# Kernel tuning notes

Measured on AMD Instinct MI355X. Metric: run time of the kernel, lower is better.

The kernel has to match this reference:

```python
import jax, jax.numpy as jnp
import numpy as np

N_NODES = 25000
N_EDGES = 400000
IN_DIM, HID_DIM, OUT_DIM = 174, 128, 64


def setup_inputs() -> dict:
    key = jax.random.key(0)
    ks = jax.random.split(key, 8)
    x = jax.random.normal(ks[0], (N_NODES, IN_DIM), dtype=jnp.float32)
    edge_index = jax.random.randint(ks[1], (2, N_EDGES), 0, N_NODES, dtype=jnp.int64)
    # PyG SAGEConv params: lin_l (neighbors, with bias), lin_r (root, no bias)
    def glorot(k, shape):
        lim = float(np.sqrt(6.0 / (shape[0] + shape[1])))
        return jax.random.uniform(k, shape, jnp.float32, -lim, lim)
    W1_l = glorot(ks[2], (HID_DIM, IN_DIM))
    W1_r = glorot(ks[3], (HID_DIM, IN_DIM))
    b1 = jnp.zeros((HID_DIM,), jnp.float32)
    W2_l = glorot(ks[4], (OUT_DIM, HID_DIM))
    W2_r = glorot(ks[5], (OUT_DIM, HID_DIM))
    b2 = jnp.zeros((OUT_DIM,), jnp.float32)
    return {"x": x, "edge_index": edge_index, "W1_l": W1_l, "b1": b1,
            "W1_r": W1_r, "W2_l": W2_l, "b2": b2, "W2_r": W2_r}


def _sage_conv(h, src, dst, W_l, b, W_r):
    # mean-aggregate neighbor features at destination nodes
    msg = h[src]                                       # [E, F] gather
    summed = jax.ops.segment_sum(msg, dst, num_segments=N_NODES)  # [N, F]
    deg = jax.ops.segment_sum(jnp.ones((src.shape[0],), h.dtype), dst,
                              num_segments=N_NODES)    # [N]
    mean = summed / jnp.maximum(deg, 1.0)[:, None]
    # out = lin_l(mean) + lin_r(h)
    return mean @ W_l.T + b + h @ W_r.T


def reference(x, edge_index, W1_l, b1, W1_r, W2_l, b2, W2_r):
    src, dst = edge_index[0], edge_index[1]
    h = _sage_conv(x, src, dst, W1_l, b1, W1_r)
    h = jax.nn.relu(h)
    # dropout is identity in eval mode (module exposes freeze() for inference)
    out = _sage_conv(h, src, dst, W2_l, b2, W2_r)
    return out
```

## Files before the change

### kernel.cpp

```cpp
#include <hip/hip_runtime.h>

#define N_NODES 25000
#define N_EDGES 400000
#define IN_DIM 174
#define HID_DIM 128
#define OUT_DIM 64
#define MPAD 25088
#define BINCAP 64

using u32 = unsigned int;
typedef __attribute__((ext_vector_type(8))) short s16x8;
typedef __attribute__((ext_vector_type(4))) float f32x4;
typedef __attribute__((ext_vector_type(4))) u32 u32x4;

__device__ __forceinline__ float bflo(u32 u) { u32 t = u << 16; return __builtin_bit_cast(float, t); }
__device__ __forceinline__ float bfhi(u32 u) { u32 t = u & 0xffff0000u; return __builtin_bit_cast(float, t); }
__device__ __forceinline__ u32 f2b(float f) {
    u32 u = __builtin_bit_cast(u32, f);
    return (u + 0x7fffu + ((u >> 16) & 1u)) >> 16;
}
__device__ __forceinline__ u32 packbf2(float a, float b) { return f2b(a) | (f2b(b) << 16); }

__device__ __forceinline__ void gload_lds16(const void* g, void* l) {
    __builtin_amdgcn_global_load_lds(
        (const __attribute__((address_space(1))) u32*)g,
        (__attribute__((address_space(3))) u32*)l, 16, 0, 0);
}

#define WB1_CNT (256 * 96)
#define WB2_CNT (128 * 64)
#define PREP_TOT (WB1_CNT + WB2_CNT + N_NODES)

__global__ __launch_bounds__(256) void prep_w_kernel(
    const float* __restrict__ W1l, const float* __restrict__ W1r,
    const float* __restrict__ W2l, const float* __restrict__ W2r,
    u32* __restrict__ wb1, u32* __restrict__ wb2, int* __restrict__ degI) {
    int idx = blockIdx.x * blockDim.x + threadIdx.x;
    if (idx < WB1_CNT) {
        int nrow = idx / 96, d2 = idx - nrow * 96;
        const float* src = (nrow < 128) ? W1l + (size_t)nrow * IN_DIM
                                        : W1r + (size_t)(nrow - 128) * IN_DIM;
        float2 v = make_float2(0.f, 0.f);
        if (d2 < 87) v = ((const float2*)src)[d2];
        wb1[idx] = packbf2(v.x, v.y);
        return;
    }
    idx -= WB1_CNT;
    if (idx < WB2_CNT) {
        int nrow = idx >> 6, d2 = idx & 63;
        const float* src = (nrow < 64) ? W2l + (size_t)nrow * HID_DIM
                                       : W2r + (size_t)(nrow - 64) * HID_DIM;
        float2 v = ((const float2*)src)[d2];
        wb2[idx] = packbf2(v.x, v.y);
        return;
    }
    idx -= WB2_CNT;
    if (idx < N_NODES) degI[idx] = 0;
}

#define G1_GEMM_BLOCKS 392
#define G1_EDGE_BLOCKS ((N_EDGES / 4 + 255) / 256)

__global__ __launch_bounds__(256) void gemm1_fused_kernel(
    const float* __restrict__ x, const ushort* __restrict__ wb1,
    ushort* __restrict__ y1n, ushort* __restrict__ y1r,
    const int* __restrict__ ei, int* __restrict__ degI, int* __restrict__ bins) {
    const int bid = blockIdx.x;
    const int tid = threadIdx.x;

    if (bid >= G1_GEMM_BLOCKS) {
        int e4 = ((bid - G1_GEMM_BLOCKS) * 256 + tid) * 4;
        if (e4 < N_EDGES) {
            int4 s = *(const int4*)(ei + e4);
            int4 t = *(const int4*)(ei + N_EDGES + e4);
            int p0 = atomicAdd(&degI[t.x], 1);
            if (p0 < BINCAP) bins[t.x * BINCAP + p0] = s.x;
            int p1 = atomicAdd(&degI[t.y], 1);
            if (p1 < BINCAP) bins[t.y * BINCAP + p1] = s.y;
            int p2 = atomicAdd(&degI[t.z], 1);
            if (p2 < BINCAP) bins[t.z * BINCAP + p2] = s.z;
            int p3 = atomicAdd(&degI[t.w], 1);
            if (p3 < BINCAP) bins[t.w * BINCAP + p3] = s.w;
        }
        return;
    }

    __shared__ ushort As[128 * 32];
    __shared__ ushort Bs[128 * 32];
    const int lane = tid & 63, w = tid >> 6;
    const int gy = bid / 196, gx = bid - gy * 196;
    const int m0 = gx * 128, n0 = gy * 128;
    const int wmo = (w >> 1) * 64;
    const int wno = (w & 1) * 64;

    f32x4 acc[4][4] = {};

    const int arow = lane >> 2;
    const int achunk = (lane & 3) * 8;
    const int r4 = tid >> 2;
    const int q  = tid & 3;

    for (int kk = 0; kk < 192; kk += 32) {
        #pragma unroll
        for (int c = 0; c < 2; ++c) {
            int r = w * 32 + c * 16;
            gload_lds16(wb1 + (size_t)(n0 + r + arow) * 192 + kk + achunk, &Bs[r * 32]);
        }
        #pragma unroll
        for (int it = 0; it < 2; ++it) {
            int r = it * 64 + r4;
            int gm = m0 + r;
            int c0 = kk + q * 8;
            u32x4 o;
            #pragma unroll
            for (int e = 0; e < 4; ++e) {
                int col = c0 + e * 2;
                float2 v = make_float2(0.f, 0.f);
                if (gm < N_NODES && col < IN_DIM)
                    v = *(const float2*)(x + (size_t)gm * IN_DIM + col);
                o[e] = packbf2(v.x, v.y);
            }
            ((u32x4*)As)[r * 4 + q] = o;
        }
        __syncthreads();
        s16x8 af[4], bf[4];
        const int fr = lane & 15, fo = (lane >> 4) * 8;
        #pragma unroll
        for (int i = 0; i < 4; ++i) {
            af[i] = *(const s16x8*)&As[(wmo + i * 16 + fr) * 32 + fo];
            bf[i] = *(const s16x8*)&Bs[(wno + i * 16 + fr) * 32 + fo];
        }
        #pragma unroll
        for (int i = 0; i < 4; ++i)
            #pragma unroll
            for (int j = 0; j < 4; ++j)
                acc[i][j] = __builtin_amdgcn_mfma_f32_16x16x32_bf16(af[i], bf[j], acc[i][j], 0, 0, 0);
        __syncthreads();
    }

    const int cr = (lane >> 4) * 4, cc = lane & 15;
    #pragma unroll
    for (int i = 0; i < 4; ++i)
        #pragma unroll
        for (int r = 0; r < 4; ++r) {
            int row = m0 + wmo + i * 16 + cr + r;
            #pragma unroll
            for (int j = 0; j < 4; ++j) {
                int colg = n0 + wno + j * 16 + cc;
                ushort* Cp = (colg < 128) ? y1n : y1r;
                int c = colg & 127;
                Cp[(size_t)row * 128 + c] = (ushort)f2b(acc[i][j][r]);
            }
        }
}

template <int K, int NSPLIT, int BM>
__global__ __launch_bounds__(256) void gemm_mfma(const ushort* __restrict__ A,
                                                 const ushort* __restrict__ B,
                                                 ushort* __restrict__ Cn,
                                                 ushort* __restrict__ Cr) {
    constexpr int MI = BM / 32;
    __shared__ ushort As[BM * 32];
    __shared__ ushort Bs[128 * 32];
    const int tid = threadIdx.x;
    const int lane = tid & 63, w = tid >> 6;
    const int m0 = blockIdx.x * BM;
    const int n0 = blockIdx.y * 128;
    const int wmo = (w >> 1) * (MI * 16);
    const int wno = (w & 1) * 64;

    f32x4 acc[MI][4] = {};

    const int arow = lane >> 2;
    const int achunk = (lane & 3) * 8;

    for (int kk = 0; kk < K; kk += 32) {
        #pragma unroll
        for (int c = 0; c < BM / 64; ++c) {
            int r = w * (BM / 4) + c * 16;
            gload_lds16(A + (size_t)(m0 + r + arow) * K + kk + achunk, &As[r * 32]);
        }
        #pragma unroll
        for (int c = 0; c < 2; ++c) {
            int r = w * 32 + c * 16;
            gload_lds16(B + (size_t)(n0 + r + arow) * K + kk + achunk, &Bs[r * 32]);
        }
        __syncthreads();
        s16x8 af[MI], bf[4];
        const int fr = lane & 15, fo = (lane >> 4) * 8;
        #pragma unroll
        for (int i = 0; i < MI; ++i)
            af[i] = *(const s16x8*)&As[(wmo + i * 16 + fr) * 32 + fo];
        #pragma unroll
        for (int j = 0; j < 4; ++j)
            bf[j] = *(const s16x8*)&Bs[(wno + j * 16 + fr) * 32 + fo];
        #pragma unroll
        for (int i = 0; i < MI; ++i)
            #pragma unroll
            for (int j = 0; j < 4; ++j)
                acc[i][j] = __builtin_amdgcn_mfma_f32_16x16x32_bf16(af[i], bf[j], acc[i][j], 0, 0, 0);
        __syncthreads();
    }

    const int cr = (lane >> 4) * 4, cc = lane & 15;
    #pragma unroll
    for (int i = 0; i < MI; ++i)
        #pragma unroll
        for (int r = 0; r < 4; ++r) {
            int row = m0 + wmo + i * 16 + cr + r;
            #pragma unroll
            for (int j = 0; j < 4; ++j) {
                int colg = n0 + wno + j * 16 + cc;
                ushort* Cp = (colg < NSPLIT) ? Cn : Cr;
                int c = (colg < NSPLIT) ? colg : colg - NSPLIT;
                Cp[(size_t)row * NSPLIT + c] = (ushort)f2b(acc[i][j][r]);
            }
        }
}

__global__ __launch_bounds__(256) void agg1_kernel(const u32* __restrict__ y1n,
                                                   const u32* __restrict__ y1r,
                                                   const int* __restrict__ degI,
                                                   const int* __restrict__ bins,
                                                   const float* __restrict__ b1,
                                                   u32* __restrict__ h1) {
    int w = threadIdx.x >> 6, lane = threadIdx.x & 63;
    int n = blockIdx.x * 4 + w;
    if (n >= N_NODES) return;
    int deg = degI[n];
    int d = min(deg, BINCAP);
    const int* bp = bins + n * BINCAP;
    float a0 = 0.f, a1 = 0.f;
    int j = 0;
    for (; j + 8 <= d; j += 8) {
        int4 sa = *(const int4*)(bp + j);
        int4 sb = *(const int4*)(bp + j + 4);
        u32 u0 = y1n[(size_t)sa.x * 64 + lane];
        u32 u1 = y1n[(size_t)sa.y * 64 + lane];
        u32 u2 = y1n[(size_t)sa.z * 64 + lane];
        u32 u3 = y1n[(size_t)sa.w * 64 + lane];
        u32 u4 = y1n[(size_t)sb.x * 64 + lane];
        u32 u5 = y1n[(size_t)sb.y * 64 + lane];
        u32 u6 = y1n[(size_t)sb.z * 64 + lane];
        u32 u7 = y1n[(size_t)sb.w * 64 + lane];
        a0 += bflo(u0) + bflo(u1) + bflo(u2) + bflo(u3)
            + bflo(u4) + bflo(u5) + bflo(u6) + bflo(u7);
        a1 += bfhi(u0) + bfhi(u1) + bfhi(u2) + bfhi(u3)
            + bfhi(u4) + bfhi(u5) + bfhi(u6) + bfhi(u7);
    }
    if (j + 4 <= d) {
        int4 s4 = *(const int4*)(bp + j);
        u32 u0 = y1n[(size_t)s4.x * 64 + lane];
        u32 u1 = y1n[(size_t)s4.y * 64 + lane];
        u32 u2 = y1n[(size_t)s4.z * 64 + lane];
        u32 u3 = y1n[(size_t)s4.w * 64 + lane];
        a0 += bflo(u0) + bflo(u1) + bflo(u2) + bflo(u3);
        a1 += bfhi(u0) + bfhi(u1) + bfhi(u2) + bfhi(u3);
        j += 4;
    }
    for (; j < d; ++j) {
        int s = bp[j];
        u32 u = y1n[(size_t)s * 64 + lane];
        a0 += bflo(u); a1 += bfhi(u);
    }
    float inv = 1.f / fmaxf((float)deg, 1.f);
    u32 ur = y1r[(size_t)n * 64 + lane];
    float2 bb = ((const float2*)b1)[lane];
    float v0 = fmaxf(a0 * inv + bflo(ur) + bb.x, 0.f);
    float v1 = fmaxf(a1 * inv + bfhi(ur) + bb.y, 0.f);
    h1[(size_t)n * 64 + lane] = packbf2(v0, v1);
}

__global__ __launch_bounds__(256) void agg2_kernel(const u32* __restrict__ y2n,
                                                   const u32* __restrict__ y2r,
                                                   const int* __restrict__ degI,
                                                   const int* __restrict__ bins,
                                                   const float* __restrict__ b2,
                                                   float2* __restrict__ out) {
    int w = threadIdx.x >> 6, lane = threadIdx.x & 63;
    int half = lane >> 5, dd = lane & 31;
    int n = blockIdx.x * 4 + w;
    if (n >= N_NODES) return;
    int deg = degI[n];
    int d = min(deg, BINCAP);
    const int* bp = bins + n * BINCAP;
    float a0 = 0.f, a1 = 0.f;
    int j = 0;
    for (; j + 8 <= d; j += 8) {
        int s0 = bp[j + half],     s1 = bp[j + 2 + half];
        int s2 = bp[j + 4 + half], s3 = bp[j + 6 + half];
        u32 u0 = y2n[(size_t)s0 * 32 + dd];
        u32 u1 = y2n[(size_t)s1 * 32 + dd];
        u32 u2 = y2n[(size_t)s2 * 32 + dd];
        u32 u3 = y2n[(size_t)s3 * 32 + dd];
        a0 += bflo(u0) + bflo(u1) + bflo(u2) + bflo(u3);
        a1 += bfhi(u0) + bfhi(u1) + bfhi(u2) + bfhi(u3);
    }
    if (j + 4 <= d) {
        int s0 = bp[j + half], s1 = bp[j + 2 + half];
        u32 u0 = y2n[(size_t)s0 * 32 + dd];
        u32 u1 = y2n[(size_t)s1 * 32 + dd];
        a0 += bflo(u0) + bflo(u1);
        a1 += bfhi(u0) + bfhi(u1);
        j += 4;
    }
    if (j + 2 <= d) {
        int s = bp[j + half];
        u32 u = y2n[(size_t)s * 32 + dd];
        a0 += bflo(u); a1 += bfhi(u);
        j += 2;
    }
    if (j < d && half == 0) {
        int s = bp[j];
        u32 u = y2n[(size_t)s * 32 + dd];
        a0 += bflo(u); a1 += bfhi(u);
    }
    a0 += __shfl_xor(a0, 32, 64);
    a1 += __shfl_xor(a1, 32, 64);
    if (half == 0) {
        float inv = 1.f / fmaxf((float)deg, 1.f);
        u32 ur = y2r[(size_t)n * 32 + dd];
        float2 bb = ((const float2*)b2)[dd];
        float2 o;
        o.x = a0 * inv + bflo(ur) + bb.x;
        o.y = a1 * inv + bfhi(ur) + bb.y;
        out[(size_t)n * 32 + dd] = o;
    }
}


extern "C" void kernel_launch(void* const* d_in, const int* in_sizes, int n_in,
                              void* d_out, int out_size, void* d_ws, size_t ws_size,
                              hipStream_t stream) {
    const float* x   = (const float*)d_in[0];
    const int*   ei  = (const int*)d_in[1];
    const float* W1l = (const float*)d_in[2];
    const float* b1  = (const float*)d_in[3];
    const float* W1r = (const float*)d_in[4];
    const float* W2l = (const float*)d_in[5];
    const float* b2  = (const float*)d_in[6];
    const float* W2r = (const float*)d_in[7];

    char* w = (char*)d_ws;
    auto alloc = [&](size_t bytes) -> char* {
        char* p = w;
        w += (bytes + 255) & ~(size_t)255;
        return p;
    };
    int* degI = (int*)alloc((size_t)N_NODES * 4);
    int* bins = (int*)alloc((size_t)N_NODES * BINCAP * 4);
    u32* wb1  = (u32*)alloc((size_t)WB1_CNT * 4);
    u32* wb2  = (u32*)alloc((size_t)WB2_CNT * 4);
    u32* y1n  = (u32*)alloc((size_t)MPAD * 64 * 4);
    u32* y1r  = (u32*)alloc((size_t)MPAD * 64 * 4);
    u32* h1   = (u32*)alloc((size_t)MPAD * 64 * 4);
    u32* y2n  = (u32*)alloc((size_t)MPAD * 32 * 4);
    u32* y2r  = (u32*)alloc((size_t)MPAD * 32 * 4);

    prep_w_kernel<<<(PREP_TOT + 255) / 256, 256, 0, stream>>>(
        W1l, W1r, W2l, W2r, wb1, wb2, degI);
    gemm1_fused_kernel<<<G1_GEMM_BLOCKS + G1_EDGE_BLOCKS, 256, 0, stream>>>(
        x, (const ushort*)wb1, (ushort*)y1n, (ushort*)y1r, ei, degI, bins);
    agg1_kernel<<<(N_NODES + 3) / 4, 256, 0, stream>>>(y1n, y1r, degI, bins, b1, h1);
    gemm_mfma<128, 64, 64><<<dim3(392, 1), 256, 0, stream>>>(
        (const ushort*)h1, (const ushort*)wb2, (ushort*)y2n, (ushort*)y2r);
    agg2_kernel<<<(N_NODES + 3) / 4, 256, 0, stream>>>(y2n, y2r, degI, bins, b2, (float2*)d_out);
}
```

Measured before the change: 80.93 us.

## Fuse layer-1 mean aggregation into the layer-2 GEMM kernel

Replaces the separate agg1 kernel and layer-2 GEMM with one kernel. Each 64-row block first gathers and averages neighbor features for its 16 rows per wave, applying bias and ReLU. It writes the bf16 result into an XOR-swizzled LDS tile, then runs the MFMA GEMM against all of W2 preloaded into LDS. This removes the h1 global round trip and one launch. The cost is much less parallelism for the latency-bound gather: 392 blocks each walking 16 nodes per wave serially, instead of thousands of one-node waves, plus 48KB of LDS per block.

```diff
diff --git a/kernel.cpp b/kernel.cpp
--- a/kernel.cpp
+++ b/kernel.cpp
@@ -90,15 +90,14 @@
     const int lane = tid & 63, w = tid >> 6;
     const int gy = bid / 196, gx = bid - gy * 196;
     const int m0 = gx * 128, n0 = gy * 128;
-    const int wmo = (w >> 1) * 64;
-    const int wno = (w & 1) * 64;
-
-    f32x4 acc[4][4] = {};
-
+    const int wmo = (w >> 1) * 64, wno = (w & 1) * 64;
     const int arow = lane >> 2;
     const int achunk = (lane & 3) * 8;
     const int r4 = tid >> 2;
     const int q  = tid & 3;
+    const int fr = lane & 15, fo = (lane >> 4) * 8;
+
+    f32x4 acc[4][4] = {};
 
     for (int kk = 0; kk < 192; kk += 32) {
         #pragma unroll
@@ -110,11 +109,10 @@
         for (int it = 0; it < 2; ++it) {
             int r = it * 64 + r4;
             int gm = m0 + r;
-            int c0 = kk + q * 8;
             u32x4 o;
             #pragma unroll
             for (int e = 0; e < 4; ++e) {
-                int col = c0 + e * 2;
+                int col = kk + q * 8 + e * 2;
                 float2 v = make_float2(0.f, 0.f);
                 if (gm < N_NODES && col < IN_DIM)
                     v = *(const float2*)(x + (size_t)gm * IN_DIM + col);
@@ -124,7 +122,6 @@
         }
         __syncthreads();
         s16x8 af[4], bf[4];
-        const int fr = lane & 15, fo = (lane >> 4) * 8;
         #pragma unroll
         for (int i = 0; i < 4; ++i) {
             af[i] = *(const s16x8*)&As[(wmo + i * 16 + fr) * 32 + fo];
@@ -154,121 +151,115 @@
         }
 }
 
-template <int K, int NSPLIT, int BM>
-__global__ __launch_bounds__(256) void gemm_mfma(const ushort* __restrict__ A,
-                                                 const ushort* __restrict__ B,
-                                                 ushort* __restrict__ Cn,
-                                                 ushort* __restrict__ Cr) {
-    constexpr int MI = BM / 32;
-    __shared__ ushort As[BM * 32];
-    __shared__ ushort Bs[128 * 32];
-    const int tid = threadIdx.x;
-    const int lane = tid & 63, w = tid >> 6;
-    const int m0 = blockIdx.x * BM;
-    const int n0 = blockIdx.y * 128;
-    const int wmo = (w >> 1) * (MI * 16);
-    const int wno = (w & 1) * 64;
-
-    f32x4 acc[MI][4] = {};
-
-    const int arow = lane >> 2;
-    const int achunk = (lane & 3) * 8;
-
-    for (int kk = 0; kk < K; kk += 32) {
-        #pragma unroll
-        for (int c = 0; c < BM / 64; ++c) {
-            int r = w * (BM / 4) + c * 16;
-            gload_lds16(A + (size_t)(m0 + r + arow) * K + kk + achunk, &As[r * 32]);
-        }
+__global__ __launch_bounds__(256) void agg1gemm2_kernel(
+    const u32* __restrict__ y1n, const u32* __restrict__ y1r,
+    const int* __restrict__ degI, const int* __restrict__ bins,
+    const float* __restrict__ b1, const ushort* __restrict__ wb2,
+    ushort* __restrict__ y2n, ushort* __restrict__ y2r) {
+    __shared__ u32 As2[64 * 64];
+    __shared__ ushort Bs2[4][128 * 32];
+    const int tid = threadIdx.x, lane = tid & 63, w = tid >> 6;
+    const int m0 = blockIdx.x * 64;
+    const int arow = lane >> 2, achunk = (lane & 3) * 8;
+
+    #pragma unroll
+    for (int ks = 0; ks < 4; ++ks)
         #pragma unroll
         for (int c = 0; c < 2; ++c) {
             int r = w * 32 + c * 16;
-            gload_lds16(B + (size_t)(n0 + r + arow) * K + kk + achunk, &Bs[r * 32]);
-        }
-        __syncthreads();
-        s16x8 af[MI], bf[4];
-        const int fr = lane & 15, fo = (lane >> 4) * 8;
-        #pragma unroll
-        for (int i = 0; i < MI; ++i)
-            af[i] = *(const s16x8*)&As[(wmo + i * 16 + fr) * 32 + fo];
+            gload_lds16(wb2 + (size_t)(r + arow) * 128 + ks * 32 + achunk,
+                        &Bs2[ks][r * 32]);
+        }
+
+    float2 bb = ((const float2*)b1)[lane];
+    for (int t = 0; t < 16; ++t) {
+        int rl = w * 16 + t;
+        int n = m0 + rl;
+        u32 val = 0;
+        if (n < N_NODES) {
+            int deg = degI[n];
+            int d = min(deg, BINCAP);
+            const int* bp = bins + n * BINCAP;
+            float a0 = 0.f, a1 = 0.f;
+            int j = 0;
+            for (; j + 8 <= d; j += 8) {
+                int4 sa = *(const int4*)(bp + j);
+                int4 sb = *(const int4*)(bp + j + 4);
+                u32 u0 = y1n[(size_t)sa.x * 64 + lane];
+                u32 u1 = y1n[(size_t)sa.y * 64 + lane];
+                u32 u2 = y1n[(size_t)sa.z * 64 + lane];
+                u32 u3 = y1n[(size_t)sa.w * 64 + lane];
+                u32 u4 = y1n[(size_t)sb.x * 64 + lane];
+                u32 u5 = y1n[(size_t)sb.y * 64 + lane];
+                u32 u6 = y1n[(size_t)sb.z * 64 + lane];
+                u32 u7 = y1n[(size_t)sb.w * 64 + lane];
+                a0 += bflo(u0) + bflo(u1) + bflo(u2) + bflo(u3)
+                    + bflo(u4) + bflo(u5) + bflo(u6) + bflo(u7);
+                a1 += bfhi(u0) + bfhi(u1) + bfhi(u2) + bfhi(u3)
+                    + bfhi(u4) + bfhi(u5) + bfhi(u6) + bfhi(u7);
+            }
+            if (j + 4 <= d) {
+                int4 s4 = *(const int4*)(bp + j);
+                u32 u0 = y1n[(size_t)s4.x * 64 + lane];
+                u32 u1 = y1n[(size_t)s4.y * 64 + lane];
+                u32 u2 = y1n[(size_t)s4.z * 64 + lane];
+                u32 u3 = y1n[(size_t)s4.w * 64 + lane];
+                a0 += bflo(u0) + bflo(u1) + bflo(u2) + bflo(u3);
+                a1 += bfhi(u0) + bfhi(u1) + bfhi(u2) + bfhi(u3);
+                j += 4;
+            }
+            for (; j < d; ++j) {
+                int s = bp[j];
+                u32 u = y1n[(size_t)s * 64 + lane];
+                a0 += bflo(u); a1 += bfhi(u);
+            }
+            float inv = 1.f / fmaxf((float)deg, 1.f);
+            u32 ur = y1r[(size_t)n * 64 + lane];
+            float v0 = fmaxf(a0 * inv + bflo(ur) + bb.x, 0.f);
+            float v1 = fmaxf(a1 * inv + bfhi(ur) + bb.y, 0.f);
+            val = packbf2(v0, v1);
+        }
+        u32 bidx = (((u32)(rl * 256 + lane * 4)) ^ (u32)((rl & 7) << 4)) >> 2;
+        As2[bidx] = val;
+    }
+    __syncthreads();
+
+    const int wmo = (w >> 1) * 32, wno = (w & 1) * 64;
+    const int fr = lane & 15, fo = (lane >> 4) * 8;
+    f32x4 acc[2][4] = {};
+    #pragma unroll
+    for (int ks = 0; ks < 4; ++ks) {
+        s16x8 af[2], bf[4];
+        #pragma unroll
+        for (int i = 0; i < 2; ++i) {
+            int mr = wmo + i * 16 + fr;
+            u32 byt = ((u32)(mr * 256 + (ks * 32 + fo) * 2)) ^ (u32)((mr & 7) << 4);
+            af[i] = *(const s16x8*)((const char*)As2 + byt);
+        }
         #pragma unroll
         for (int j = 0; j < 4; ++j)
-            bf[j] = *(const s16x8*)&Bs[(wno + j * 16 + fr) * 32 + fo];
-        #pragma unroll
-        for (int i = 0; i < MI; ++i)
+            bf[j] = *(const s16x8*)&Bs2[ks][(wno + j * 16 + fr) * 32 + fo];
+        #pragma unroll
+        for (int i = 0; i < 2; ++i)
             #pragma unroll
             for (int j = 0; j < 4; ++j)
                 acc[i][j] = __builtin_amdgcn_mfma_f32_16x16x32_bf16(af[i], bf[j], acc[i][j], 0, 0, 0);
-        __syncthreads();
     }
 
     const int cr = (lane >> 4) * 4, cc = lane & 15;
     #pragma unroll
-    for (int i = 0; i < MI; ++i)
+    for (int i = 0; i < 2; ++i)
         #pragma unroll
         for (int r = 0; r < 4; ++r) {
             int row = m0 + wmo + i * 16 + cr + r;
             #pragma unroll
             for (int j = 0; j < 4; ++j) {
-                int colg = n0 + wno + j * 16 + cc;
-                ushort* Cp = (colg < NSPLIT) ? Cn : Cr;
-                int c = (colg < NSPLIT) ? colg : colg - NSPLIT;
-                Cp[(size_t)row * NSPLIT + c] = (ushort)f2b(acc[i][j][r]);
-            }
-        }
-}
-
-__global__ __launch_bounds__(256) void agg1_kernel(const u32* __restrict__ y1n,
-                                                   const u32* __restrict__ y1r,
-                                                   const int* __restrict__ degI,
-                                                   const int* __restrict__ bins,
-                                                   const float* __restrict__ b1,
-                                                   u32* __restrict__ h1) {
-    int w = threadIdx.x >> 6, lane = threadIdx.x & 63;
-    int n = blockIdx.x * 4 + w;
-    if (n >= N_NODES) return;
-    int deg = degI[n];
-    int d = min(deg, BINCAP);
-    const int* bp = bins + n * BINCAP;
-    float a0 = 0.f, a1 = 0.f;
-    int j = 0;
-    for (; j + 8 <= d; j += 8) {
-        int4 sa = *(const int4*)(bp + j);
-        int4 sb = *(const int4*)(bp + j + 4);
-        u32 u0 = y1n[(size_t)sa.x * 64 + lane];
-        u32 u1 = y1n[(size_t)sa.y * 64 + lane];
-        u32 u2 = y1n[(size_t)sa.z * 64 + lane];
-        u32 u3 = y1n[(size_t)sa.w * 64 + lane];
-        u32 u4 = y1n[(size_t)sb.x * 64 + lane];
-        u32 u5 = y1n[(size_t)sb.y * 64 + lane];
-        u32 u6 = y1n[(size_t)sb.z * 64 + lane];
-        u32 u7 = y1n[(size_t)sb.w * 64 + lane];
-        a0 += bflo(u0) + bflo(u1) + bflo(u2) + bflo(u3)
-            + bflo(u4) + bflo(u5) + bflo(u6) + bflo(u7);
-        a1 += bfhi(u0) + bfhi(u1) + bfhi(u2) + bfhi(u3)
-            + bfhi(u4) + bfhi(u5) + bfhi(u6) + bfhi(u7);
-    }
-    if (j + 4 <= d) {
-        int4 s4 = *(const int4*)(bp + j);
-        u32 u0 = y1n[(size_t)s4.x * 64 + lane];
-        u32 u1 = y1n[(size_t)s4.y * 64 + lane];
-        u32 u2 = y1n[(size_t)s4.z * 64 + lane];
-        u32 u3 = y1n[(size_t)s4.w * 64 + lane];
-        a0 += bflo(u0) + bflo(u1) + bflo(u2) + bflo(u3);
-        a1 += bfhi(u0) + bfhi(u1) + bfhi(u2) + bfhi(u3);
-        j += 4;
-    }
-    for (; j < d; ++j) {
-        int s = bp[j];
-        u32 u = y1n[(size_t)s * 64 + lane];
-        a0 += bflo(u); a1 += bfhi(u);
-    }
-    float inv = 1.f / fmaxf((float)deg, 1.f);
-    u32 ur = y1r[(size_t)n * 64 + lane];
-    float2 bb = ((const float2*)b1)[lane];
-    float v0 = fmaxf(a0 * inv + bflo(ur) + bb.x, 0.f);
-    float v1 = fmaxf(a1 * inv + bfhi(ur) + bb.y, 0.f);
-    h1[(size_t)n * 64 + lane] = packbf2(v0, v1);
+                int colg = wno + j * 16 + cc;
+                ushort* Cp = (colg < 64) ? y2n : y2r;
+                int c = colg & 63;
+                Cp[(size_t)row * 64 + c] = (ushort)f2b(acc[i][j][r]);
+            }
+        }
 }
 
 __global__ __launch_bounds__(256) void agg2_kernel(const u32* __restrict__ y2n,
@@ -341,10 +332,10 @@
     const float* b2  = (const float*)d_in[6];
     const float* W2r = (const float*)d_in[7];
 
-    char* w = (char*)d_ws;
+    char* wp = (char*)d_ws;
     auto alloc = [&](size_t bytes) -> char* {
-        char* p = w;
-        w += (bytes + 255) & ~(size_t)255;
+        char* p = wp;
+        wp += (bytes + 255) & ~(size_t)255;
         return p;
     };
     int* degI = (int*)alloc((size_t)N_NODES * 4);
@@ -353,7 +344,6 @@
     u32* wb2  = (u32*)alloc((size_t)WB2_CNT * 4);
     u32* y1n  = (u32*)alloc((size_t)MPAD * 64 * 4);
     u32* y1r  = (u32*)alloc((size_t)MPAD * 64 * 4);
-    u32* h1   = (u32*)alloc((size_t)MPAD * 64 * 4);
     u32* y2n  = (u32*)alloc((size_t)MPAD * 32 * 4);
     u32* y2r  = (u32*)alloc((size_t)MPAD * 32 * 4);
 
@@ -361,8 +351,8 @@
         W1l, W1r, W2l, W2r, wb1, wb2, degI);
     gemm1_fused_kernel<<<G1_GEMM_BLOCKS + G1_EDGE_BLOCKS, 256, 0, stream>>>(
         x, (const ushort*)wb1, (ushort*)y1n, (ushort*)y1r, ei, degI, bins);
-    agg1_kernel<<<(N_NODES + 3) / 4, 256, 0, stream>>>(y1n, y1r, degI, bins, b1, h1);
-    gemm_mfma<128, 64, 64><<<dim3(392, 1), 256, 0, stream>>>(
-        (const ushort*)h1, (const ushort*)wb2, (ushort*)y2n, (ushort*)y2r);
-    agg2_kernel<<<(N_NODES + 3) / 4, 256, 0, stream>>>(y2n, y2r, degI, bins, b2, (float2*)d_out);
-}
+    agg1gemm2_kernel<<<392, 256, 0, stream>>>(
+        y1n, y1r, degI, bins, b1, (const ushort*)wb2, (ushort*)y2n, (ushort*)y2r);
+    agg2_kernel<<<(N_NODES + 3) / 4, 256, 0, stream>>>(
+        y2n, y2r, degI, bins, b2, (float2*)d_out);
+}
```

Result: slower. 109.6 us (+35.5%).
